# Kernel tuning notes

Measured on AMD Instinct MI355X. Metric: run time of the kernel, lower is better.

## Reference

```python
import jax, jax.numpy as jnp
import numpy as np

L, E, H, D, F, B, CIN, N = 12, 128, 4, 32, 512, 64, 256, 257


def setup_inputs() -> dict:
    key = jax.random.key(0)
    ks = jax.random.split(key, 10)
    s = 0.02
    rn = lambda k, shape: jax.random.normal(k, shape, jnp.float32) * s
    return {
        "feat": jax.random.normal(ks[0], (B, CIN, 32, 32), jnp.float32),
        "conv_w": rn(ks[1], (E, CIN, 3, 3)),
        "conv_b": jnp.zeros((E,), jnp.float32),
        "pos_emb": rn(ks[2], (1, N, E)),
        "cls_token": rn(ks[3], (1, 1, E)),
        "ln1_s": jnp.ones((L, E), jnp.float32),
        "ln1_b": jnp.zeros((L, E), jnp.float32),
        "qkv_w": rn(ks[4], (L, 3 * E, E)),
        "qkv_b": jnp.zeros((L, 3 * E), jnp.float32),
        "proj_w": rn(ks[5], (L, E, E)),
        "proj_b": jnp.zeros((L, E), jnp.float32),
        "ln2_s": jnp.ones((L, E), jnp.float32),
        "ln2_b": jnp.zeros((L, E), jnp.float32),
        "ffn1_w": rn(ks[6], (L, F, E)),
        "ffn1_b": jnp.zeros((L, F), jnp.float32),
        "ffn2_w": rn(ks[7], (L, E, F)),
        "ffn2_b": jnp.zeros((L, E), jnp.float32),
        "fn_s": jnp.ones((E,), jnp.float32),
        "fn_b": jnp.zeros((E,), jnp.float32),
        "fc_w": rn(ks[8], (2, E)),
        "fc_b": jnp.zeros((2,), jnp.float32),
    }


def _ln(x, s, b, eps):
    m = jnp.mean(x, -1, keepdims=True)
    v = jnp.mean((x - m) ** 2, -1, keepdims=True)
    return (x - m) * jax.lax.rsqrt(v + eps) * s + b


def reference(feat, conv_w, conv_b, pos_emb, cls_token, ln1_s, ln1_b, qkv_w,
              qkv_b, proj_w, proj_b, ln2_s, ln2_b, ffn1_w, ffn1_b, ffn2_w,
              ffn2_b, fn_s, fn_b, fc_w, fc_b):
    # patch embed: 3x3 conv stride 2 -> 16x16 = 256 tokens
    emb = jax.lax.conv_general_dilated(
        feat, conv_w, (2, 2), ((1, 1), (1, 1)),
        dimension_numbers=("NCHW", "OIHW", "NCHW")) + conv_b[None, :, None, None]
    Bsz = emb.shape[0]
    emb = emb.reshape(Bsz, E, -1).transpose(0, 2, 1)  # [B, 256, E]
    x = jnp.concatenate([jnp.broadcast_to(cls_token, (Bsz, 1, E)), emb], axis=1)
    x = x + pos_emb  # [B, N, E]
    scale = (E // H) ** -0.5

    def block(x, p):
        l1s, l1b, qw, qb, pw, pb, l2s, l2b, w1, b1, w2, b2 = p
        h = _ln(x, l1s, l1b, 1e-5)
        qkv = (h @ qw.T + qb).reshape(Bsz, N, 3, H, D).transpose(2, 0, 3, 1, 4)
        q, k, v = qkv[0], qkv[1], qkv[2]  # [B, H, N, D]
        att = jax.nn.softmax(jnp.einsum("bhnd,bhmd->bhnm", q, k) * scale, axis=-1)
        o = jnp.einsum("bhnm,bhmd->bhnd", att, v).transpose(0, 2, 1, 3).reshape(Bsz, N, E)
        x = x + (o @ pw.T + pb)
        h2 = _ln(x, l2s, l2b, 1e-5)
        x = x + (jax.nn.gelu(h2 @ w1.T + b1, approximate=False) @ w2.T + b2)
        return x, None

    x, _ = jax.lax.scan(block, x, (ln1_s, ln1_b, qkv_w, qkv_b, proj_w, proj_b,
                                   ln2_s, ln2_b, ffn1_w, ffn1_b, ffn2_w, ffn2_b))
    x = _ln(x, fn_s, fn_b, 1e-6)
    out_feat = x[:, 0, :]
    out = out_feat @ fc_w.T + fc_b
    return (out, out_feat)
```

## Files before the change

kernel.cpp:

```cpp
#include <hip/hip_runtime.h>
#include <math.h>

constexpr int NP_ = 272;
constexpr int MP_ = 64 * NP_;
constexpr int TPB_ = 17;

typedef short short8 __attribute__((ext_vector_type(8)));
typedef float f32x4 __attribute__((ext_vector_type(4)));

__device__ inline short f2bs(float f) {
    unsigned u = __builtin_bit_cast(unsigned, f);
    unsigned r = (u + 0x7fffu + ((u >> 16) & 1u)) >> 16;
    return (short)r;
}

__device__ inline f32x4 mfma16(short8 a, short8 b, f32x4 c) {
    return __builtin_amdgcn_mfma_f32_16x16x32_bf16(a, b, c, 0, 0, 0);
}

__global__ void repack_all(const float* __restrict__ qkvw, const float* __restrict__ projw,
                           const float* __restrict__ f1w, const float* __restrict__ f2w,
                           const float* __restrict__ convw,
                           short* __restrict__ wq, short* __restrict__ wp,
                           short* __restrict__ w1, short* __restrict__ w2,
                           short* __restrict__ wc) {
    int o = blockIdx.x * 256 + threadIdx.x;
    if (o < 589824) {
        int l = o / 49152, r = o % 49152;
        int chunk = r / 3072, w = r % 3072;
        int n = w >> 3, k = chunk * 8 + (w & 7);
        wq[o] = f2bs(qkvw[(size_t)l * 49152 + n * 128 + k]);
        return;
    }
    o -= 589824;
    if (o < 196608) {
        int l = o / 16384, r = o % 16384;
        int chunk = r / 1024, w = r % 1024;
        int n = w >> 3, k = chunk * 8 + (w & 7);
        wp[o] = f2bs(projw[(size_t)l * 16384 + n * 128 + k]);
        return;
    }
    o -= 196608;
    if (o < 786432) {
        int l = o / 65536, r = o % 65536;
        int chunk = r / 4096, w = r % 4096;
        int n = w >> 3, k = chunk * 8 + (w & 7);
        w1[o] = f2bs(f1w[(size_t)l * 65536 + n * 128 + k]);
        return;
    }
    o -= 786432;
    if (o < 786432) {
        int l = o / 65536, r = o % 65536;
        int chunk = r / 1024, w = r % 1024;
        int n = w >> 3, k = chunk * 8 + (w & 7);
        w2[o] = f2bs(f2w[(size_t)l * 65536 + n * 512 + k]);
        return;
    }
    o -= 786432;
    if (o < 294912) {
        int j = o & 7;
        int col = (o >> 3) & 127;
        int c = o >> 10;
        int qd = c & 3, cscb = c >> 2;
        int cs = cscb & 7, kykx = cscb >> 3;
        int cin = cs * 32 + qd * 8 + j;
        int ky = kykx / 3, kx = kykx % 3;
        wc[o] = f2bs(convw[((col * 256 + cin) * 3 + ky) * 3 + kx]);
    }
}

__global__ __launch_bounds__(256) void feat_nhwc(const float* __restrict__ feat, short* __restrict__ fp) {
    __shared__ float tile[32][33];
    int b = blockIdx.x >> 5, y = blockIdx.x & 31;
    int t = threadIdx.x;
    for (int c0 = 0; c0 < 256; c0 += 32) {
        int ci = t >> 5, x = t & 31;
        for (int cc = ci; cc < 32; cc += 8)
            tile[cc][x] = feat[((size_t)(b * 256 + c0 + cc) * 32 + y) * 32 + x];
        __syncthreads();
        for (int i = t; i < 1024; i += 256) {
            int c = i & 31, x2 = i >> 5;
            fp[((size_t)(b * 34 + y + 1) * 34 + x2 + 1) * 256 + c0 + c] = f2bs(tile[c][x2]);
        }
        __syncthreads();
    }
    short* rowp = fp + (size_t)(b * 34 + y + 1) * 34 * 256;
    for (int c = t; c < 256; c += 256) { rowp[c] = 0; rowp[33 * 256 + c] = 0; }
    if (y == 0) {
        short* r0 = fp + (size_t)(b * 34) * 34 * 256;
        for (int i = t; i < 34 * 256; i += 256) r0[i] = 0;
    }
    if (y == 31) {
        short* r33 = fp + (size_t)(b * 34 + 33) * 34 * 256;
        for (int i = t; i < 34 * 256; i += 256) r33[i] = 0;
    }
}

__global__ __launch_bounds__(256) void conv_gemm(const short* __restrict__ fp, const short* __restrict__ wr,
                                                 const float* __restrict__ cb, const float* __restrict__ pos,
                                                 float* __restrict__ X) {
    __shared__ __align__(16) short Ain[3 * 34 * 256];
    int b = blockIdx.x >> 4, oy = blockIdx.x & 15;
    int tid = threadIdx.x;
    for (int idx = tid; idx < 3 * 34 * 32; idx += 256) {
        int r = idx / 1088, rem = idx - r * 1088;
        int x = rem >> 5, c = rem & 31;
        short8 v = *(const short8*)(fp + ((size_t)(b * 34 + 2 * oy + r) * 34 + x) * 256 + c * 8);
        *(short8*)(Ain + (r * 34 + x) * 256 + ((c ^ ((x >> 1) & 7)) * 8)) = v;
    }
    __syncthreads();
    int wave = tid >> 6, lane = tid & 63;
    int ng = wave, lo = lane & 15, qd = lane >> 4;
    f32x4 acc[2] = {};
#pragma unroll
    for (int ky = 0; ky < 3; ++ky)
#pragma unroll
        for (int kx = 0; kx < 3; ++kx) {
            int sx = 2 * lo + kx;
            int arow = (ky * 34 + sx) * 256;
            int sw = (sx >> 1) & 7;
            const short* wb = wr + (((size_t)((ky * 3 + kx) * 8) * 4 + qd) * 128 + ng * 32 + lo) * 8;
#pragma unroll
            for (int cs = 0; cs < 8; ++cs) {
                short8 af = *(const short8*)(Ain + arow + (((cs * 4 + qd) ^ sw) * 8));
                short8 b0 = *(const short8*)(wb + (size_t)cs * 4096);
                short8 b1 = *(const short8*)(wb + (size_t)cs * 4096 + 128);
                acc[0] = mfma16(af, b0, acc[0]);
                acc[1] = mfma16(af, b1, acc[1]);
            }
        }
#pragma unroll
    for (int t = 0; t < 2; ++t) {
        int e = ng * 32 + t * 16 + lo;
        float bias = cb[e];
#pragma unroll
        for (int r = 0; r < 4; ++r) {
            int tok = 1 + oy * 16 + qd * 4 + r;
            X[((size_t)b * NP_ + tok) * 128 + e] = acc[t][r] + bias + pos[tok * 128 + e];
        }
    }
}

__global__ __launch_bounds__(256) void cls_init(const float* __restrict__ cls, const float* __restrict__ pos,
                                                float* __restrict__ X) {
    int b = blockIdx.x, tid = threadIdx.x;
    if (tid < 128) X[(size_t)b * NP_ * 128 + tid] = cls[tid] + pos[tid];
    for (int idx = tid; idx < 15 * 128; idx += 256)
        X[((size_t)b * NP_ + 257) * 128 + idx] = 0.f;
}

__device__ inline void ln_tile16(const float* Xl, const float* __restrict__ s, const float* __restrict__ bb,
                                 short* SB, int tid, float eps) {
    int wv = tid >> 6, lane = tid & 63;
    int r4 = lane & 3, c32 = lane >> 2;
    int row = wv * 4 + r4;
    const float* xr = Xl + row * 132 + c32 * 8;
    float4 a = *(const float4*)(xr);
    float4 b = *(const float4*)(xr + 4);
    float v[8] = {a.x, a.y, a.z, a.w, b.x, b.y, b.z, b.w};
    float sum = v[0] + v[1] + v[2] + v[3] + v[4] + v[5] + v[6] + v[7];
    sum += __shfl_xor(sum, 4); sum += __shfl_xor(sum, 8);
    sum += __shfl_xor(sum, 16); sum += __shfl_xor(sum, 32);
    float mean = sum * (1.f / 128.f);
    float vs = 0.f;
#pragma unroll
    for (int j = 0; j < 8; ++j) { float d = v[j] - mean; vs += d * d; }
    vs += __shfl_xor(vs, 4); vs += __shfl_xor(vs, 8);
    vs += __shfl_xor(vs, 16); vs += __shfl_xor(vs, 32);
    float rs = rsqrtf(vs * (1.f / 128.f) + eps);
    float4 s0 = *(const float4*)(s + c32 * 8), s1 = *(const float4*)(s + c32 * 8 + 4);
    float4 b0 = *(const float4*)(bb + c32 * 8), b1 = *(const float4*)(bb + c32 * 8 + 4);
    float sv[8] = {s0.x, s0.y, s0.z, s0.w, s1.x, s1.y, s1.z, s1.w};
    float bv[8] = {b0.x, b0.y, b0.z, b0.w, b1.x, b1.y, b1.z, b1.w};
    short8 o;
#pragma unroll
    for (int j = 0; j < 8; ++j) o[j] = f2bs((v[j] - mean) * rs * sv[j] + bv[j]);
    *(short8*)(SB + (c32 * 16 + row) * 8) = o;
}

__device__ inline void qkv_stage16(const short* SB, const short* __restrict__ wq, const float* __restrict__ qb,
                                   int mg, int wv, int lo, int qd,
                                   short* __restrict__ Qf, short* __restrict__ Kf, short* __restrict__ Vt) {
    int n0 = wv * 96;
    f32x4 acc[6] = {};
#pragma unroll
    for (int ki = 0; ki < 4; ++ki) {
        int kq = ki * 4 + qd;
        short8 a = *(const short8*)(SB + (kq * 16 + lo) * 8);
#pragma unroll
        for (int t = 0; t < 6; ++t) {
            short8 bf = *(const short8*)(wq + ((size_t)kq * 384 + n0 + t * 16 + lo) * 8);
            acc[t] = mfma16(a, bf, acc[t]);
        }
    }
#pragma unroll
    for (int t = 0; t < 6; ++t) {
        int n = n0 + t * 16 + lo;
        float bvv = qb[n];
        int seg = n >> 7, m = n & 127, h = m >> 5, d = m & 31;
#pragma unroll
        for (int r = 0; r < 4; ++r) {
            int row = mg * 16 + qd * 4 + r;
            int bb2 = row / NP_, q = row - bb2 * NP_;
            short val = f2bs(acc[t][r] + bvv);
            if (seg == 2)
                Vt[((size_t)(bb2 * 4 + h) * 32 + d) * NP_ + q] = val;
            else
                (seg ? Kf : Qf)[((size_t)(bb2 * 4 + h) * 4 + (d >> 3)) * (NP_ * 8) + q * 8 + (d & 7)] = val;
        }
    }
}

__global__ __launch_bounds__(256, 4) void qkv0(const float* __restrict__ X, const short* __restrict__ wq,
                                               const float* __restrict__ qb, const float* __restrict__ ls,
                                               const float* __restrict__ lb,
                                               short* __restrict__ Qf, short* __restrict__ Kf,
                                               short* __restrict__ Vt) {
    __shared__ __align__(16) float Xl[16 * 132];
    __shared__ __align__(16) short SB[2048];
    int mg = blockIdx.x, tid = threadIdx.x;
    for (int idx = tid; idx < 512; idx += 256) {
        int tok = idx >> 5, c = idx & 31;
        *(float4*)(Xl + tok * 132 + c * 4) = *(const float4*)(X + (size_t)(mg * 16 + tok) * 128 + c * 4);
    }
    __syncthreads();
    ln_tile16(Xl, ls, lb, SB, tid, 1e-5f);
    __syncthreads();
    int wv = tid >> 6, lane = tid & 63;
    qkv_stage16(SB, wq, qb, mg, wv, lane & 15, lane >> 4, Qf, Kf, Vt);
}

template <int LAST>
__global__ __launch_bounds__(256, 4) void layer_tail(
    const short* __restrict__ Of, const short* __restrict__ wp, const float* __restrict__ pb,
    const float* __restrict__ l2s, const float* __restrict__ l2b,
    const short* __restrict__ w1, const float* __restrict__ b1,
    const short* __restrict__ w2, const float* __restrict__ b2,
    float* __restrict__ X,
    const float* __restrict__ l1s, const float* __restrict__ l1b,
    const short* __restrict__ wq, const float* __restrict__ qb,
    short* __restrict__ Qf, short* __restrict__ Kf, short* __restrict__ Vt) {
    __shared__ __align__(16) short SB[2048];
    __shared__ __align__(16) float Xl[16 * 132];
    __shared__ __align__(16) short Uh[32 * 136];
    int mg = blockIdx.x, tid = threadIdx.x;
    const short* osrc = Of + (size_t)mg * 2048;
    for (int idx = tid; idx < 256; idx += 256)
        *(short8*)(SB + idx * 8) = *(const short8*)(osrc + idx * 8);
    for (int idx = tid; idx < 512; idx += 256) {
        int tok = idx >> 5, c = idx & 31;
        *(float4*)(Xl + tok * 132 + c * 4) = *(const float4*)(X + (size_t)(mg * 16 + tok) * 128 + c * 4);
    }
    __syncthreads();
    int wv = tid >> 6, lane = tid & 63, lo = lane & 15, qd = lane >> 4;
    {
        int n0 = wv * 32;
        f32x4 pa[2] = {};
#pragma unroll
        for (int ki = 0; ki < 4; ++ki) {
            int kq = ki * 4 + qd;
            short8 a = *(const short8*)(SB + (kq * 16 + lo) * 8);
            short8 b0 = *(const short8*)(wp + ((size_t)kq * 128 + n0 + lo) * 8);
            short8 b1 = *(const short8*)(wp + ((size_t)kq * 128 + n0 + 16 + lo) * 8);
            pa[0] = mfma16(a, b0, pa[0]);
            pa[1] = mfma16(a, b1, pa[1]);
        }
        float pb0 = pb[n0 + lo], pb1 = pb[n0 + 16 + lo];
#pragma unroll
        for (int r = 0; r < 4; ++r) {
            Xl[(qd * 4 + r) * 132 + n0 + lo] += pa[0][r] + pb0;
            Xl[(qd * 4 + r) * 132 + n0 + 16 + lo] += pa[1][r] + pb1;
        }
    }
    __syncthreads();
    ln_tile16(Xl, l2s, l2b, SB, tid, 1e-5f);
    __syncthreads();
    f32x4 facc[2] = {};
#pragma unroll
    for (int hh = 0; hh < 2; ++hh) {
        {
            int n0h = wv * 64;
            f32x4 fa[4] = {};
#pragma unroll
            for (int ki = 0; ki < 4; ++ki) {
                int kq = ki * 4 + qd;
                short8 a = *(const short8*)(SB + (kq * 16 + lo) * 8);
#pragma unroll
                for (int t = 0; t < 4; ++t) {
                    short8 bf = *(const short8*)(w1 + ((size_t)kq * 512 + hh * 256 + n0h + t * 16 + lo) * 8);
                    fa[t] = mfma16(a, bf, fa[t]);
                }
            }
#pragma unroll
            for (int t = 0; t < 4; ++t) {
                int nl = n0h + t * 16 + lo;
                float bvv = b1[hh * 256 + nl];
#pragma unroll
                for (int r = 0; r < 4; ++r) {
                    float x = fa[t][r] + bvv;
                    float u = x * (0.7978845608f + 0.0356774081f * x * x);
                    x = x / (1.f + __expf(-2.f * u));
                    Uh[(nl >> 3) * 136 + (qd * 4 + r) * 8 + (nl & 7)] = f2bs(x);
                }
            }
        }
        __syncthreads();
        {
            int n0 = wv * 32;
#pragma unroll
            for (int ki = 0; ki < 8; ++ki) {
                int kq2 = ki * 4 + qd;
                short8 a = *(const short8*)(Uh + kq2 * 136 + lo * 8);
                short8 b0 = *(const short8*)(w2 + (((size_t)(hh * 32 + kq2)) * 128 + n0 + lo) * 8);
                short8 b1 = *(const short8*)(w2 + (((size_t)(hh * 32 + kq2)) * 128 + n0 + 16 + lo) * 8);
                facc[0] = mfma16(a, b0, facc[0]);
                facc[1] = mfma16(a, b1, facc[1]);
            }
        }
        if (hh == 0) __syncthreads();
    }
    {
        int n0 = wv * 32;
        float b20 = b2[n0 + lo], b21 = b2[n0 + 16 + lo];
#pragma unroll
        for (int r = 0; r < 4; ++r) {
            Xl[(qd * 4 + r) * 132 + n0 + lo] += facc[0][r] + b20;
            Xl[(qd * 4 + r) * 132 + n0 + 16 + lo] += facc[1][r] + b21;
        }
    }
    __syncthreads();
    for (int idx = tid; idx < 512; idx += 256) {
        int tok = idx >> 5, c = idx & 31;
        *(float4*)(X + (size_t)(mg * 16 + tok) * 128 + c * 4) = *(const float4*)(Xl + tok * 132 + c * 4);
    }
    if (LAST) return;
    ln_tile16(Xl, l1s, l1b, SB, tid, 1e-5f);
    __syncthreads();
    qkv_stage16(SB, wq, qb, mg, wv, lo, qd, Qf, Kf, Vt);
}

__global__ __launch_bounds__(256, 4) void attn(const short* __restrict__ Qf, const short* __restrict__ Kf,
                                               const short* __restrict__ Vt, short* __restrict__ Of) {
    __shared__ __align__(16) short Vl[32 * 296];
    __shared__ __align__(16) short Pl[4][544];
    int b = blockIdx.x >> 3, h = (blockIdx.x >> 1) & 3, half = blockIdx.x & 1;
    int tid = threadIdx.x;
    const short* kf = Kf + (size_t)(b * 4 + h) * (4 * NP_ * 8);
    const short* qf = Qf + (size_t)(b * 4 + h) * (4 * NP_ * 8);
    const short* vt = Vt + (size_t)(b * 4 + h) * (32 * NP_);
    for (int idx = tid; idx < 32 * 37; idx += 256) {
        int d = idx / 37, c8 = idx - d * 37;
        short8 v = {};
        if (c8 < 34) v = *(const short8*)(vt + d * NP_ + c8 * 8);
        *(short8*)(Vl + d * 296 + c8 * 8) = v;
    }
    __syncthreads();
    int wv = tid >> 6, lane = tid & 63, lo = lane & 15, qd = lane >> 4;
    short* Pw = Pl[wv];
    const float scale = 0.17677669529663687f;
    for (int it = 0; it < 3; ++it) {
        int qt = it * 8 + half * 4 + wv;
        if (qt > 16) break;
        short8 qfr = *(const short8*)(qf + ((size_t)qd * NP_ + qt * 16 + lo) * 8);
        f32x4 sc[17];
#pragma unroll
        for (int kt = 0; kt < 17; ++kt) {
            short8 kfr = *(const short8*)(kf + ((size_t)qd * NP_ + kt * 16 + lo) * 8);
            f32x4 z = {};
            sc[kt] = mfma16(qfr, kfr, z);
        }
        float mx[4] = {-1e30f, -1e30f, -1e30f, -1e30f};
#pragma unroll
        for (int kt = 0; kt < 17; ++kt) {
            bool valid = (kt * 16 + lo) < 257;
#pragma unroll
            for (int r = 0; r < 4; ++r) {
                float v2 = valid ? sc[kt][r] * scale : -1e30f;
                sc[kt][r] = v2;
                mx[r] = fmaxf(mx[r], v2);
            }
        }
#pragma unroll
        for (int r = 0; r < 4; ++r) {
            mx[r] = fmaxf(mx[r], __shfl_xor(mx[r], 1));
            mx[r] = fmaxf(mx[r], __shfl_xor(mx[r], 2));
            mx[r] = fmaxf(mx[r], __shfl_xor(mx[r], 4));
            mx[r] = fmaxf(mx[r], __shfl_xor(mx[r], 8));
        }
        float l[4] = {0.f, 0.f, 0.f, 0.f};
#pragma unroll
        for (int kt = 0; kt < 17; ++kt)
#pragma unroll
            for (int r = 0; r < 4; ++r) {
                float p = __expf(sc[kt][r] - mx[r]);
                sc[kt][r] = p;
                l[r] += p;
            }
#pragma unroll
        for (int r = 0; r < 4; ++r) {
            l[r] += __shfl_xor(l[r], 1);
            l[r] += __shfl_xor(l[r], 2);
            l[r] += __shfl_xor(l[r], 4);
            l[r] += __shfl_xor(l[r], 8);
        }
        float rl[4];
#pragma unroll
        for (int r = 0; r < 4; ++r) rl[r] = 1.f / l[r];
        f32x4 oa[2] = {};
#pragma unroll
        for (int ks = 0; ks < 9; ++ks) {
#pragma unroll
            for (int kt2 = 0; kt2 < 2; ++kt2) {
                int kt = ks * 2 + kt2;
                int lkey = kt2 * 16 + lo;
#pragma unroll
                for (int r = 0; r < 4; ++r) {
                    short pv = (kt < 17) ? f2bs(sc[kt][r] * rl[r]) : (short)0;
                    Pw[(lkey >> 3) * 128 + (qd * 4 + r) * 8 + (lkey & 7)] = pv;
                }
            }
            short8 pf = *(const short8*)(Pw + (qd * 16 + lo) * 8);
#pragma unroll
            for (int nt = 0; nt < 2; ++nt) {
                short8 vfr = *(const short8*)(Vl + (nt * 16 + lo) * 296 + ks * 32 + qd * 8);
                oa[nt] = mfma16(pf, vfr, oa[nt]);
            }
        }
        int tile = b * TPB_ + qt;
#pragma unroll
        for (int nt = 0; nt < 2; ++nt)
#pragma unroll
            for (int r = 0; r < 4; ++r) {
                int qq = qt * 16 + qd * 4 + r;
                if (qq <= 256) {
                    int col = h * 32 + nt * 16 + lo;
                    Of[(size_t)tile * 2048 + (col >> 3) * 128 + (qd * 4 + r) * 8 + (col & 7)] = f2bs(oa[nt][r]);
                }
            }
    }
}

__global__ __launch_bounds__(64) void final_head(const float* __restrict__ X, const float* __restrict__ fs,
                                                 const float* __restrict__ fb, const float* __restrict__ fcw,
                                                 const float* __restrict__ fcb, float* __restrict__ out) {
    int b = blockIdx.x, lane = threadIdx.x;
    float2 v = *(const float2*)(X + (size_t)b * NP_ * 128 + lane * 2);
    float sum = v.x + v.y;
#pragma unroll
    for (int m = 1; m < 64; m <<= 1) sum += __shfl_xor(sum, m);
    float mean = sum * (1.f / 128.f);
    float d0 = v.x - mean, d1 = v.y - mean;
    float vs = d0 * d0 + d1 * d1;
#pragma unroll
    for (int m = 1; m < 64; m <<= 1) vs += __shfl_xor(vs, m);
    float rs = rsqrtf(vs * (1.f / 128.f) + 1e-6f);
    int e = lane * 2;
    float f0 = d0 * rs * fs[e] + fb[e];
    float f1 = d1 * rs * fs[e + 1] + fb[e + 1];
    out[128 + b * 128 + e] = f0;
    out[128 + b * 128 + e + 1] = f1;
    float p0 = f0 * fcw[e] + f1 * fcw[e + 1];
    float p1 = f0 * fcw[128 + e] + f1 * fcw[128 + e + 1];
#pragma unroll
    for (int m = 1; m < 64; m <<= 1) {
        p0 += __shfl_xor(p0, m);
        p1 += __shfl_xor(p1, m);
    }
    if (lane == 0) {
        out[b * 2 + 0] = p0 + fcb[0];
        out[b * 2 + 1] = p1 + fcb[1];
    }
}

extern "C" void kernel_launch(void* const* d_in, const int* in_sizes, int n_in,
                              void* d_out, int out_size, void* d_ws, size_t ws_size,
                              hipStream_t stream) {
    const float* feat    = (const float*)d_in[0];
    const float* conv_w  = (const float*)d_in[1];
    const float* conv_b  = (const float*)d_in[2];
    const float* pos_emb = (const float*)d_in[3];
    const float* cls_tok = (const float*)d_in[4];
    const float* ln1_s   = (const float*)d_in[5];
    const float* ln1_b   = (const float*)d_in[6];
    const float* qkv_w   = (const float*)d_in[7];
    const float* qkv_b   = (const float*)d_in[8];
    const float* proj_w  = (const float*)d_in[9];
    const float* proj_b  = (const float*)d_in[10];
    const float* ln2_s   = (const float*)d_in[11];
    const float* ln2_b   = (const float*)d_in[12];
    const float* ffn1_w  = (const float*)d_in[13];
    const float* ffn1_b  = (const float*)d_in[14];
    const float* ffn2_w  = (const float*)d_in[15];
    const float* ffn2_b  = (const float*)d_in[16];
    const float* fn_s    = (const float*)d_in[17];
    const float* fn_b    = (const float*)d_in[18];
    const float* fc_w    = (const float*)d_in[19];
    const float* fc_b    = (const float*)d_in[20];

    char* p = (char*)d_ws;
    auto alloc = [&](size_t bytes) { char* r = p; p += (bytes + 255) & ~(size_t)255; return r; };
    short* wq  = (short*)alloc((size_t)589824 * 2);
    short* wp  = (short*)alloc((size_t)196608 * 2);
    short* w1  = (short*)alloc((size_t)786432 * 2);
    short* w2  = (short*)alloc((size_t)786432 * 2);
    short* wc  = (short*)alloc((size_t)294912 * 2);
    short* fpd = (short*)alloc((size_t)64 * 34 * 34 * 256 * 2);
    float* X   = (float*)alloc((size_t)MP_ * 128 * 4);
    short* Qf  = (short*)alloc((size_t)64 * 16 * NP_ * 8 * 2);
    short* Kf  = (short*)alloc((size_t)64 * 16 * NP_ * 8 * 2);
    short* Vt  = (short*)alloc((size_t)64 * 4 * 32 * NP_ * 2);
    short* Of  = (short*)alloc((size_t)(MP_ / 16) * 2048 * 2);

    repack_all<<<10368, 256, 0, stream>>>(qkv_w, proj_w, ffn1_w, ffn2_w, conv_w, wq, wp, w1, w2, wc);
    feat_nhwc<<<64 * 32, 256, 0, stream>>>(feat, fpd);
    conv_gemm<<<1024, 256, 0, stream>>>(fpd, wc, conv_b, pos_emb, X);
    cls_init<<<64, 256, 0, stream>>>(cls_tok, pos_emb, X);

    qkv0<<<1088, 256, 0, stream>>>(X, wq, qkv_b, ln1_s, ln1_b, Qf, Kf, Vt);
    for (int l = 0; l < 12; ++l) {
        attn<<<512, 256, 0, stream>>>(Qf, Kf, Vt, Of);
        if (l < 11)
            layer_tail<0><<<1088, 256, 0, stream>>>(Of, wp + (size_t)l * 16384, proj_b + l * 128,
                                                    ln2_s + l * 128, ln2_b + l * 128,
                                                    w1 + (size_t)l * 65536, ffn1_b + l * 512,
                                                    w2 + (size_t)l * 65536, ffn2_b + l * 128, X,
                                                    ln1_s + (l + 1) * 128, ln1_b + (l + 1) * 128,
                                                    wq + (size_t)(l + 1) * 49152, qkv_b + (l + 1) * 384,
                                                    Qf, Kf, Vt);
        else
            layer_tail<1><<<1088, 256, 0, stream>>>(Of, wp + (size_t)l * 16384, proj_b + l * 128,
                                                    ln2_s + l * 128, ln2_b + l * 128,
                                                    w1 + (size_t)l * 65536, ffn1_b + l * 512,
                                                    w2 + (size_t)l * 65536, ffn2_b + l * 128, X,
                                                    ln1_s, ln1_b, wq, qkv_b, Qf, Kf, Vt);
    }
    final_head<<<64, 64, 0, stream>>>(X, fn_s, fn_b, fc_w, fc_b, (float*)d_out);
}
```

Before: 864.2 us.

## Prefetch weight fragments across barriers, split attention into quarters, fold cls init into conv

Issues the first global weight-fragment loads of each GEMM stage (proj, FFN1 halves, FFN2 halves, next-layer QKV) before the preceding __syncthreads or LayerNorm, so their latency overlaps other work. The FFN loop is manually unrolled into two halves so loads for the second half can start early. Attention now launches 1024 blocks, each taking four query tiles, with one block also handling the leftover tile 16, instead of 512 blocks looping up to three times. The cls_init kernel is folded into conv_gemm to remove a launch. Costs are more registers held across barriers, which may lower occupancy, and each attention block reloading V into LDS for less work.

```diff
diff --git a/kernel.cpp b/kernel.cpp
--- a/kernel.cpp
+++ b/kernel.cpp
@@ -98,7 +98,7 @@
 
 __global__ __launch_bounds__(256) void conv_gemm(const short* __restrict__ fp, const short* __restrict__ wr,
                                                  const float* __restrict__ cb, const float* __restrict__ pos,
-                                                 float* __restrict__ X) {
+                                                 const float* __restrict__ cls, float* __restrict__ X) {
     __shared__ __align__(16) short Ain[3 * 34 * 256];
     int b = blockIdx.x >> 4, oy = blockIdx.x & 15;
     int tid = threadIdx.x;
@@ -139,14 +139,11 @@
             X[((size_t)b * NP_ + tok) * 128 + e] = acc[t][r] + bias + pos[tok * 128 + e];
         }
     }
-}
-
-__global__ __launch_bounds__(256) void cls_init(const float* __restrict__ cls, const float* __restrict__ pos,
-                                                float* __restrict__ X) {
-    int b = blockIdx.x, tid = threadIdx.x;
-    if (tid < 128) X[(size_t)b * NP_ * 128 + tid] = cls[tid] + pos[tid];
-    for (int idx = tid; idx < 15 * 128; idx += 256)
-        X[((size_t)b * NP_ + 257) * 128 + idx] = 0.f;
+    if (oy == 0) {
+        if (tid < 128) X[(size_t)b * NP_ * 128 + tid] = cls[tid] + pos[tid];
+        for (int idx = tid; idx < 15 * 128; idx += 256)
+            X[((size_t)b * NP_ + 257) * 128 + idx] = 0.f;
+    }
 }
 
 __device__ inline void ln_tile16(const float* Xl, const float* __restrict__ s, const float* __restrict__ bb,
@@ -179,7 +176,7 @@
 }
 
 __device__ inline void qkv_stage16(const short* SB, const short* __restrict__ wq, const float* __restrict__ qb,
-                                   int mg, int wv, int lo, int qd,
+                                   const short8* pre, int mg, int wv, int lo, int qd,
                                    short* __restrict__ Qf, short* __restrict__ Kf, short* __restrict__ Vt) {
     int n0 = wv * 96;
     f32x4 acc[6] = {};
@@ -189,7 +186,8 @@
         short8 a = *(const short8*)(SB + (kq * 16 + lo) * 8);
 #pragma unroll
         for (int t = 0; t < 6; ++t) {
-            short8 bf = *(const short8*)(wq + ((size_t)kq * 384 + n0 + t * 16 + lo) * 8);
+            short8 bf = (ki == 0) ? pre[t]
+                                  : *(const short8*)(wq + ((size_t)kq * 384 + n0 + t * 16 + lo) * 8);
             acc[t] = mfma16(a, bf, acc[t]);
         }
     }
@@ -219,15 +217,19 @@
     __shared__ __align__(16) float Xl[16 * 132];
     __shared__ __align__(16) short SB[2048];
     int mg = blockIdx.x, tid = threadIdx.x;
+    int wv = tid >> 6, lane = tid & 63, lo = lane & 15, qd = lane >> 4;
     for (int idx = tid; idx < 512; idx += 256) {
         int tok = idx >> 5, c = idx & 31;
         *(float4*)(Xl + tok * 132 + c * 4) = *(const float4*)(X + (size_t)(mg * 16 + tok) * 128 + c * 4);
     }
+    short8 preq[6];
+#pragma unroll
+    for (int t = 0; t < 6; ++t)
+        preq[t] = *(const short8*)(wq + ((size_t)qd * 384 + wv * 96 + t * 16 + lo) * 8);
     __syncthreads();
     ln_tile16(Xl, ls, lb, SB, tid, 1e-5f);
     __syncthreads();
-    int wv = tid >> 6, lane = tid & 63;
-    qkv_stage16(SB, wq, qb, mg, wv, lane & 15, lane >> 4, Qf, Kf, Vt);
+    qkv_stage16(SB, wq, qb, preq, mg, wv, lo, qd, Qf, Kf, Vt);
 }
 
 template <int LAST>
@@ -244,6 +246,7 @@
     __shared__ __align__(16) float Xl[16 * 132];
     __shared__ __align__(16) short Uh[32 * 136];
     int mg = blockIdx.x, tid = threadIdx.x;
+    int wv = tid >> 6, lane = tid & 63, lo = lane & 15, qd = lane >> 4;
     const short* osrc = Of + (size_t)mg * 2048;
     for (int idx = tid; idx < 256; idx += 256)
         *(short8*)(SB + idx * 8) = *(const short8*)(osrc + idx * 8);
@@ -251,19 +254,23 @@
         int tok = idx >> 5, c = idx & 31;
         *(float4*)(Xl + tok * 132 + c * 4) = *(const float4*)(X + (size_t)(mg * 16 + tok) * 128 + c * 4);
     }
-    __syncthreads();
-    int wv = tid >> 6, lane = tid & 63, lo = lane & 15, qd = lane >> 4;
+    int n0 = wv * 32;
+    short8 prep[8];
+#pragma unroll
+    for (int ki = 0; ki < 4; ++ki) {
+        int kq = ki * 4 + qd;
+        prep[ki * 2] = *(const short8*)(wp + ((size_t)kq * 128 + n0 + lo) * 8);
+        prep[ki * 2 + 1] = *(const short8*)(wp + ((size_t)kq * 128 + n0 + 16 + lo) * 8);
+    }
+    __syncthreads();
     {
-        int n0 = wv * 32;
         f32x4 pa[2] = {};
 #pragma unroll
         for (int ki = 0; ki < 4; ++ki) {
             int kq = ki * 4 + qd;
             short8 a = *(const short8*)(SB + (kq * 16 + lo) * 8);
-            short8 b0 = *(const short8*)(wp + ((size_t)kq * 128 + n0 + lo) * 8);
-            short8 b1 = *(const short8*)(wp + ((size_t)kq * 128 + n0 + 16 + lo) * 8);
-            pa[0] = mfma16(a, b0, pa[0]);
-            pa[1] = mfma16(a, b1, pa[1]);
+            pa[0] = mfma16(a, prep[ki * 2], pa[0]);
+            pa[1] = mfma16(a, prep[ki * 2 + 1], pa[1]);
         }
         float pb0 = pb[n0 + lo], pb1 = pb[n0 + 16 + lo];
 #pragma unroll
@@ -272,55 +279,97 @@
             Xl[(qd * 4 + r) * 132 + n0 + 16 + lo] += pa[1][r] + pb1;
         }
     }
+    int n0h = wv * 64;
+    short8 pre1[4];
+#pragma unroll
+    for (int t = 0; t < 4; ++t)
+        pre1[t] = *(const short8*)(w1 + ((size_t)qd * 512 + n0h + t * 16 + lo) * 8);
     __syncthreads();
     ln_tile16(Xl, l2s, l2b, SB, tid, 1e-5f);
     __syncthreads();
     f32x4 facc[2] = {};
-#pragma unroll
-    for (int hh = 0; hh < 2; ++hh) {
-        {
-            int n0h = wv * 64;
-            f32x4 fa[4] = {};
-#pragma unroll
-            for (int ki = 0; ki < 4; ++ki) {
-                int kq = ki * 4 + qd;
-                short8 a = *(const short8*)(SB + (kq * 16 + lo) * 8);
-#pragma unroll
-                for (int t = 0; t < 4; ++t) {
-                    short8 bf = *(const short8*)(w1 + ((size_t)kq * 512 + hh * 256 + n0h + t * 16 + lo) * 8);
-                    fa[t] = mfma16(a, bf, fa[t]);
-                }
-            }
+    {
+        f32x4 fa[4] = {};
+#pragma unroll
+        for (int ki = 0; ki < 4; ++ki) {
+            int kq = ki * 4 + qd;
+            short8 a = *(const short8*)(SB + (kq * 16 + lo) * 8);
 #pragma unroll
             for (int t = 0; t < 4; ++t) {
-                int nl = n0h + t * 16 + lo;
-                float bvv = b1[hh * 256 + nl];
-#pragma unroll
-                for (int r = 0; r < 4; ++r) {
-                    float x = fa[t][r] + bvv;
-                    float u = x * (0.7978845608f + 0.0356774081f * x * x);
-                    x = x / (1.f + __expf(-2.f * u));
-                    Uh[(nl >> 3) * 136 + (qd * 4 + r) * 8 + (nl & 7)] = f2bs(x);
-                }
-            }
-        }
-        __syncthreads();
-        {
-            int n0 = wv * 32;
-#pragma unroll
-            for (int ki = 0; ki < 8; ++ki) {
-                int kq2 = ki * 4 + qd;
-                short8 a = *(const short8*)(Uh + kq2 * 136 + lo * 8);
-                short8 b0 = *(const short8*)(w2 + (((size_t)(hh * 32 + kq2)) * 128 + n0 + lo) * 8);
-                short8 b1 = *(const short8*)(w2 + (((size_t)(hh * 32 + kq2)) * 128 + n0 + 16 + lo) * 8);
-                facc[0] = mfma16(a, b0, facc[0]);
-                facc[1] = mfma16(a, b1, facc[1]);
-            }
-        }
-        if (hh == 0) __syncthreads();
-    }
+                short8 bf = (ki == 0) ? pre1[t]
+                                      : *(const short8*)(w1 + ((size_t)kq * 512 + n0h + t * 16 + lo) * 8);
+                fa[t] = mfma16(a, bf, fa[t]);
+            }
+        }
+#pragma unroll
+        for (int t = 0; t < 4; ++t) {
+            int nl = n0h + t * 16 + lo;
+            float bvv = b1[nl];
+#pragma unroll
+            for (int r = 0; r < 4; ++r) {
+                float x = fa[t][r] + bvv;
+                float u = x * (0.7978845608f + 0.0356774081f * x * x);
+                x = x / (1.f + __expf(-2.f * u));
+                Uh[(nl >> 3) * 136 + (qd * 4 + r) * 8 + (nl & 7)] = f2bs(x);
+            }
+        }
+    }
+    short8 pre2a = *(const short8*)(w2 + ((size_t)qd * 128 + n0 + lo) * 8);
+    short8 pre2b = *(const short8*)(w2 + ((size_t)qd * 128 + n0 + 16 + lo) * 8);
+    short8 pre1b[4];
+#pragma unroll
+    for (int t = 0; t < 4; ++t)
+        pre1b[t] = *(const short8*)(w1 + ((size_t)qd * 512 + 256 + n0h + t * 16 + lo) * 8);
+    __syncthreads();
+#pragma unroll
+    for (int ki = 0; ki < 8; ++ki) {
+        int kq2 = ki * 4 + qd;
+        short8 a = *(const short8*)(Uh + kq2 * 136 + lo * 8);
+        short8 b0 = (ki == 0) ? pre2a : *(const short8*)(w2 + ((size_t)kq2 * 128 + n0 + lo) * 8);
+        short8 b1 = (ki == 0) ? pre2b : *(const short8*)(w2 + ((size_t)kq2 * 128 + n0 + 16 + lo) * 8);
+        facc[0] = mfma16(a, b0, facc[0]);
+        facc[1] = mfma16(a, b1, facc[1]);
+    }
+    short8 pre3a = *(const short8*)(w2 + ((size_t)(32 + qd) * 128 + n0 + lo) * 8);
+    short8 pre3b = *(const short8*)(w2 + ((size_t)(32 + qd) * 128 + n0 + 16 + lo) * 8);
+    __syncthreads();
     {
-        int n0 = wv * 32;
+        f32x4 fa[4] = {};
+#pragma unroll
+        for (int ki = 0; ki < 4; ++ki) {
+            int kq = ki * 4 + qd;
+            short8 a = *(const short8*)(SB + (kq * 16 + lo) * 8);
+#pragma unroll
+            for (int t = 0; t < 4; ++t) {
+                short8 bf = (ki == 0) ? pre1b[t]
+                                      : *(const short8*)(w1 + ((size_t)kq * 512 + 256 + n0h + t * 16 + lo) * 8);
+                fa[t] = mfma16(a, bf, fa[t]);
+            }
+        }
+#pragma unroll
+        for (int t = 0; t < 4; ++t) {
+            int nl = n0h + t * 16 + lo;
+            float bvv = b1[256 + nl];
+#pragma unroll
+            for (int r = 0; r < 4; ++r) {
+                float x = fa[t][r] + bvv;
+                float u = x * (0.7978845608f + 0.0356774081f * x * x);
+                x = x / (1.f + __expf(-2.f * u));
+                Uh[(nl >> 3) * 136 + (qd * 4 + r) * 8 + (nl & 7)] = f2bs(x);
+            }
+        }
+    }
+    __syncthreads();
+#pragma unroll
+    for (int ki = 0; ki < 8; ++ki) {
+        int kq2 = ki * 4 + qd;
+        short8 a = *(const short8*)(Uh + kq2 * 136 + lo * 8);
+        short8 b0 = (ki == 0) ? pre3a : *(const short8*)(w2 + ((size_t)(32 + kq2) * 128 + n0 + lo) * 8);
+        short8 b1 = (ki == 0) ? pre3b : *(const short8*)(w2 + ((size_t)(32 + kq2) * 128 + n0 + 16 + lo) * 8);
+        facc[0] = mfma16(a, b0, facc[0]);
+        facc[1] = mfma16(a, b1, facc[1]);
+    }
+    {
         float b20 = b2[n0 + lo], b21 = b2[n0 + 16 + lo];
 #pragma unroll
         for (int r = 0; r < 4; ++r) {
@@ -328,6 +377,12 @@
             Xl[(qd * 4 + r) * 132 + n0 + 16 + lo] += facc[1][r] + b21;
         }
     }
+    short8 preq[6];
+    if (!LAST) {
+#pragma unroll
+        for (int t = 0; t < 6; ++t)
+            preq[t] = *(const short8*)(wq + ((size_t)qd * 384 + wv * 96 + t * 16 + lo) * 8);
+    }
     __syncthreads();
     for (int idx = tid; idx < 512; idx += 256) {
         int tok = idx >> 5, c = idx & 31;
@@ -336,14 +391,14 @@
     if (LAST) return;
     ln_tile16(Xl, l1s, l1b, SB, tid, 1e-5f);
     __syncthreads();
-    qkv_stage16(SB, wq, qb, mg, wv, lo, qd, Qf, Kf, Vt);
+    qkv_stage16(SB, wq, qb, preq, mg, wv, lo, qd, Qf, Kf, Vt);
 }
 
 __global__ __launch_bounds__(256, 4) void attn(const short* __restrict__ Qf, const short* __restrict__ Kf,
                                                const short* __restrict__ Vt, short* __restrict__ Of) {
     __shared__ __align__(16) short Vl[32 * 296];
     __shared__ __align__(16) short Pl[4][544];
-    int b = blockIdx.x >> 3, h = (blockIdx.x >> 1) & 3, half = blockIdx.x & 1;
+    int b = blockIdx.x >> 4, h = (blockIdx.x >> 2) & 3, qc = blockIdx.x & 3;
     int tid = threadIdx.x;
     const short* kf = Kf + (size_t)(b * 4 + h) * (4 * NP_ * 8);
     const short* qf = Qf + (size_t)(b * 4 + h) * (4 * NP_ * 8);
@@ -358,9 +413,10 @@
     int wv = tid >> 6, lane = tid & 63, lo = lane & 15, qd = lane >> 4;
     short* Pw = Pl[wv];
     const float scale = 0.17677669529663687f;
-    for (int it = 0; it < 3; ++it) {
-        int qt = it * 8 + half * 4 + wv;
-        if (qt > 16) break;
+    for (int it = 0; it < 2; ++it) {
+        int qt;
+        if (it == 0) qt = qc * 4 + wv;
+        else { if ((qc | wv) != 0) break; qt = 16; }
         short8 qfr = *(const short8*)(qf + ((size_t)qd * NP_ + qt * 16 + lo) * 8);
         f32x4 sc[17];
 #pragma unroll
@@ -513,12 +569,11 @@
 
     repack_all<<<10368, 256, 0, stream>>>(qkv_w, proj_w, ffn1_w, ffn2_w, conv_w, wq, wp, w1, w2, wc);
     feat_nhwc<<<64 * 32, 256, 0, stream>>>(feat, fpd);
-    conv_gemm<<<1024, 256, 0, stream>>>(fpd, wc, conv_b, pos_emb, X);
-    cls_init<<<64, 256, 0, stream>>>(cls_tok, pos_emb, X);
+    conv_gemm<<<1024, 256, 0, stream>>>(fpd, wc, conv_b, pos_emb, cls_tok, X);
 
     qkv0<<<1088, 256, 0, stream>>>(X, wq, qkv_b, ln1_s, ln1_b, Qf, Kf, Vt);
     for (int l = 0; l < 12; ++l) {
-        attn<<<512, 256, 0, stream>>>(Qf, Kf, Vt, Of);
+        attn<<<1024, 256, 0, stream>>>(Qf, Kf, Vt, Of);
         if (l < 11)
             layer_tail<0><<<1088, 256, 0, stream>>>(Of, wp + (size_t)l * 16384, proj_b + l * 128,
                                                     ln2_s + l * 128, ln2_b + l * 128,
```

Result: faster. 807.8 us (-6.5%).
